# Kernel optimization log

Measured on AMD Instinct MI355X. Metric: run time of the kernel, lower is better.

The kernel has to match this reference:

```python
import jax, jax.numpy as jnp
import numpy as np

N_NODES = 100000
N_EDGES = 1600000
D_IN = 128
D_OUT = 32


def setup_inputs() -> dict:
    key = jax.random.key(0)
    k1, k2, k3 = jax.random.split(key, 3)
    x = jax.random.normal(k1, (N_NODES, D_IN), dtype=jnp.float32)
    edge_index = jax.random.randint(k2, (2, N_EDGES), 0, N_NODES, dtype=jnp.int64)
    W = jax.random.normal(k3, (D_IN, D_OUT), dtype=jnp.float32) * (1.0 / np.sqrt(D_IN))
    b = jnp.zeros((D_OUT,), dtype=jnp.float32)
    return {"x": x, "edge_index": edge_index, "W": W, "b": b}


def gcn_conv(x, edge_index, W, b):
    n = x.shape[0]
    # add self-loops (PyG GCNConv default)
    loops = jnp.arange(n, dtype=edge_index.dtype)
    row = jnp.concatenate([edge_index[0], loops])  # source
    col = jnp.concatenate([edge_index[1], loops])  # target
    # symmetric normalization: deg computed on target of A + I
    deg = jax.ops.segment_sum(jnp.ones_like(col, dtype=x.dtype), col, num_segments=n)
    dis = jnp.where(deg > 0, jax.lax.rsqrt(deg), 0.0)
    norm = dis[row] * dis[col]  # [E+N]
    # linear transform first, then gather-scale-scatter aggregation
    xw = x @ W  # [N, D_OUT]
    msgs = norm[:, None] * xw[row]  # [E+N, D_OUT]
    out = jax.ops.segment_sum(msgs, col, num_segments=n)
    return out + b


def reference(x, edge_index, W, b):
    return gcn_conv(x, edge_index, W, b)
```

## Files before the change

kernel.cpp:

```cpp
#include <hip/hip_runtime.h>

#define NN 100000
#define NE 1600000
#define DIN 128
#define DOUT 32
#define NBUK 391
#define FILLB 512
#define CHUNK 3125
#define CAP 8192
#define NTILES 6250
#define XWB 782

typedef unsigned short ushort_t;
typedef unsigned int uint_t;
typedef _Float16 f16x8 __attribute__((ext_vector_type(8)));
typedef float f32x4 __attribute__((ext_vector_type(4)));

static __device__ __forceinline__ ushort_t f2h_u(float f) {
    _Float16 h = (_Float16)f;
    ushort_t u;
    __builtin_memcpy(&u, &h, 2);
    return u;
}
static __device__ __forceinline__ float h2f(ushort_t us) {
    _Float16 h;
    __builtin_memcpy(&h, &us, 2);
    return (float)h;
}

__global__ __launch_bounds__(512)
void wb_zero_kernel(const float* __restrict__ W, ushort_t* __restrict__ Wht,
                    int* __restrict__ bsum) {
    if (blockIdx.x < 8) {
        int i = blockIdx.x * 512 + threadIdx.x;
        int c = i >> 7, k = i & 127;
        Wht[(size_t)c * DIN + k] = f2h_u(W[(size_t)k * DOUT + c]);
    } else {
        int t = threadIdx.x;
        if (t < NBUK) bsum[t] = 0;
    }
}

__global__ __launch_bounds__(512)
void fill_xw_kernel(const int* __restrict__ row, const int* __restrict__ col,
                    int* __restrict__ histmat, int* __restrict__ bsum,
                    unsigned int* __restrict__ records,
                    const float* __restrict__ x, const ushort_t* __restrict__ Wht,
                    ushort_t* __restrict__ xwsh) {
    __shared__ unsigned int stage[CHUNK];
    __shared__ int hist[NBUK];
    __shared__ int s[512];
    __shared__ int lcur[NBUK];
    if (blockIdx.x < FILLB) {
        int t = threadIdx.x, blk = blockIdx.x;
        for (int bb = t; bb < NBUK; bb += 512) hist[bb] = 0;
        __syncthreads();
        int e0 = blk * CHUNK;
        for (int j = t; j < CHUNK; j += 512) atomicAdd(&hist[col[e0 + j] >> 8], 1);
        __syncthreads();
        int own = (t < NBUK) ? hist[t] : 0;
        s[t] = own;
        __syncthreads();
        for (int off = 1; off < 512; off <<= 1) {
            int u = (t >= off) ? s[t - off] : 0;
            __syncthreads();
            s[t] += u;
            __syncthreads();
        }
        int excl = s[t] - own;
        if (t <= NBUK) histmat[(size_t)blk * (NBUK + 1) + t] = excl;
        if (t < NBUK) {
            if (own) atomicAdd(&bsum[t], own);
            lcur[t] = excl;
        }
        __syncthreads();
        for (int j = t; j < CHUNK; j += 512) {
            int e = e0 + j;
            int c = col[e];
            int slot = atomicAdd(&lcur[c >> 8], 1);
            stage[slot] = ((unsigned int)row[e] << 8) | (unsigned int)(c & 255);
        }
        __syncthreads();
        for (int j = t; j < CHUNK; j += 512)
            records[(size_t)blk * CHUNK + j] = stage[j];
        return;
    }
    int t = threadIdx.x;
    int wv = t >> 6, lane = t & 63;
    int wtile = (blockIdx.x - FILLB) * 8 + wv;
    if (wtile >= NTILES) return;
    int r0 = wtile * 16;
    int rowi = lane & 15;
    int kg = lane >> 4;

    f16x8 bfrag[2][4];
#pragma unroll
    for (int t2 = 0; t2 < 2; ++t2)
#pragma unroll
        for (int ss = 0; ss < 4; ++ss)
            bfrag[t2][ss] = *(const f16x8*)(Wht + (size_t)(t2 * 16 + rowi) * DIN + ss * 32 + kg * 8);

    const float* __restrict__ xr = x + (size_t)(r0 + rowi) * DIN;
    float4 xa[8];
#pragma unroll
    for (int ss = 0; ss < 4; ++ss) {
        xa[2 * ss]     = *(const float4*)(xr + ss * 32 + kg * 8);
        xa[2 * ss + 1] = *(const float4*)(xr + ss * 32 + kg * 8 + 4);
    }
    f16x8 afrag[4];
#pragma unroll
    for (int ss = 0; ss < 4; ++ss) {
        f16x8 a;
        a[0] = (_Float16)xa[2 * ss].x;     a[1] = (_Float16)xa[2 * ss].y;
        a[2] = (_Float16)xa[2 * ss].z;     a[3] = (_Float16)xa[2 * ss].w;
        a[4] = (_Float16)xa[2 * ss + 1].x; a[5] = (_Float16)xa[2 * ss + 1].y;
        a[6] = (_Float16)xa[2 * ss + 1].z; a[7] = (_Float16)xa[2 * ss + 1].w;
        afrag[ss] = a;
    }

    f32x4 acc0 = {0.f, 0.f, 0.f, 0.f};
    f32x4 acc1 = {0.f, 0.f, 0.f, 0.f};
#pragma unroll
    for (int ss = 0; ss < 4; ++ss) {
        acc0 = __builtin_amdgcn_mfma_f32_16x16x32_f16(afrag[ss], bfrag[0][ss], acc0, 0, 0, 0);
        acc1 = __builtin_amdgcn_mfma_f32_16x16x32_f16(afrag[ss], bfrag[1][ss], acc1, 0, 0, 0);
    }

#pragma unroll
    for (int j = 0; j < 4; ++j) {
        int orow = r0 + kg * 4 + j;
        xwsh[(size_t)orow * DOUT + rowi]      = f2h_u(acc0[j]);
        xwsh[(size_t)orow * DOUT + 16 + rowi] = f2h_u(acc1[j]);
    }
}

__global__ __launch_bounds__(512)
void bscan_kernel(const int* __restrict__ bsum, int* __restrict__ base) {
    __shared__ int s[512];
    int t = threadIdx.x;
    int own = (t < NBUK) ? bsum[t] : 0;
    s[t] = own;
    __syncthreads();
    for (int off = 1; off < 512; off <<= 1) {
        int v = (t >= off) ? s[t - off] : 0;
        __syncthreads();
        s[t] += v;
        __syncthreads();
    }
    if (t < NBUK) {
        base[t] = s[t] - own;
        if (t == NBUK - 1) base[NBUK] = s[t];
    }
}

__global__ __launch_bounds__(512)
void sort_kernel(const int* __restrict__ base, const int* __restrict__ histmat,
                 const unsigned int* __restrict__ records,
                 int* __restrict__ srcs, float* __restrict__ dis,
                 int* __restrict__ offs, ushort_t* __restrict__ xwsh) {
    __shared__ unsigned int stage[CAP];
    __shared__ int slen[512];
    __shared__ int hist[256];
    __shared__ int sc[256];
    __shared__ int lcur[256];
    __shared__ float disL[256];
    int b = blockIdx.x, t = threadIdx.x;
    int s_off = histmat[(size_t)t * (NBUK + 1) + b];
    int e_off = histmat[(size_t)t * (NBUK + 1) + b + 1];
    int len = e_off - s_off;
    slen[t] = len;
    if (t < 256) hist[t] = 0;
    __syncthreads();
    for (int off = 1; off < 512; off <<= 1) {
        int u = (t >= off) ? slen[t - off] : 0;
        __syncthreads();
        slen[t] += u;
        __syncthreads();
    }
    int pos = slen[t] - len;
    int cnt = slen[511];

    const unsigned int* seg = records + (size_t)t * CHUNK + s_off;
    for (int k = 0; k < len; k += 8) {
        unsigned int v[8];
#pragma unroll
        for (int u = 0; u < 8; ++u) {
            int idx = (k + u < len) ? (k + u) : (len - 1);
            v[u] = seg[idx];
        }
#pragma unroll
        for (int u = 0; u < 8; ++u)
            if (k + u < len) {
                stage[pos + k + u] = v[u];
                atomicAdd(&hist[v[u] & 255u], 1);
            }
    }
    __syncthreads();

    int d = (t < 256) ? hist[t] : 0;
    if (t < 256) sc[t] = d;
    __syncthreads();
    for (int off = 1; off < 256; off <<= 1) {
        int u = (t < 256 && t >= off) ? sc[t - off] : 0;
        __syncthreads();
        if (t < 256) sc[t] += u;
        __syncthreads();
    }
    int sbase = base[b];
    if (t < 256) {
        int excl = sc[t] - d;
        float dv = rsqrtf((float)(d + 1));
        disL[t] = dv;
        int n = (b << 8) + t;
        if (n < NN) {
            dis[n] = dv;
            offs[n] = sbase + excl;
            if (n == NN - 1) offs[NN] = sbase + cnt;
        }
        lcur[t] = excl;
    }
    __syncthreads();
    for (int j = t; j < cnt; j += 512) {
        unsigned int rec = stage[j];
        int slot = atomicAdd(&lcur[rec & 255u], 1);
        srcs[sbase + slot] = (int)(rec >> 8);
    }
    int n0 = b << 8;
    for (int idx = t; idx < 256 * 16; idx += 512) {
        int loc = idx >> 4;
        int n = n0 + loc;
        if (n >= NN) break;
        uint_t* p = (uint_t*)(xwsh + ((size_t)n << 5)) + (idx & 15);
        uint_t v = *p;
        float dv = disL[loc];
        float lo = h2f((ushort_t)(v & 0xffffu)) * dv;
        float hi = h2f((ushort_t)(v >> 16)) * dv;
        *p = (uint_t)f2h_u(lo) | ((uint_t)f2h_u(hi) << 16);
    }
}

__global__ __launch_bounds__(256)
void aggregate_kernel(const int* __restrict__ offs, const int* __restrict__ srcs,
                      const float* __restrict__ dis, const ushort_t* __restrict__ xwsh,
                      const float* __restrict__ bias, float* __restrict__ out) {
    int gw = (int)((blockIdx.x * (long long)blockDim.x + threadIdx.x) >> 6);
    int half = (threadIdx.x >> 5) & 1;
    int wid = gw * 2 + half;
    if (wid >= NN) return;
    int d = threadIdx.x & 31;

    int s = offs[wid], e = offs[wid + 1];
    float acc = h2f(xwsh[((size_t)wid << 5) + d]);
    for (int i = s; i < e; i += 8) {
        int r[8];
        ushort_t u[8];
#pragma unroll
        for (int k = 0; k < 8; ++k) {
            int j = i + k;
            r[k] = srcs[j < e ? j : e - 1];
        }
#pragma unroll
        for (int k = 0; k < 8; ++k) u[k] = xwsh[((size_t)r[k] << 5) + d];
#pragma unroll
        for (int k = 0; k < 8; ++k) acc += (i + k < e) ? h2f(u[k]) : 0.f;
    }
    out[((size_t)wid << 5) + d] = dis[wid] * acc + bias[d];
}

__global__ void deg_count_kernel(const int* __restrict__ col, int* __restrict__ deg) {
    int e = blockIdx.x * blockDim.x + threadIdx.x;
    if (e < NE) atomicAdd(&deg[col[e]], 1);
}
__global__ void dis_kernel(const int* __restrict__ deg, float* __restrict__ dis) {
    int i = blockIdx.x * blockDim.x + threadIdx.x;
    if (i < NN) dis[i] = rsqrtf((float)(deg[i] + 1));
}
__global__ void xw_init_kernel(const float* __restrict__ x, const float* __restrict__ W,
                               const float* __restrict__ b, const float* __restrict__ dis,
                               float* __restrict__ xw, float* __restrict__ out) {
    __shared__ float Ws[DIN * DOUT];
    for (int i = threadIdx.x; i < DIN * DOUT; i += blockDim.x) Ws[i] = W[i];
    __syncthreads();
    int idx = blockIdx.x * blockDim.x + threadIdx.x;
    if (idx >= NN * DOUT) return;
    int n = idx >> 5;
    int d = idx & (DOUT - 1);
    const float* xr = x + (long long)n * DIN;
    float acc = 0.f;
#pragma unroll
    for (int k = 0; k < DIN; ++k) acc += xr[k] * Ws[k * DOUT + d];
    xw[idx] = acc;
    float di = dis[n];
    out[idx] = di * di * acc + b[d];
}
__global__ void scatter_kernel(const int* __restrict__ row, const int* __restrict__ col,
                               const float* __restrict__ dis, const float* __restrict__ xw,
                               float* __restrict__ out) {
    long long idx = (long long)blockIdx.x * blockDim.x + threadIdx.x;
    if (idx >= (long long)NE * DOUT) return;
    int e = (int)(idx >> 5);
    int d = (int)(idx & (DOUT - 1));
    int r = row[e];
    int c = col[e];
    atomicAdd(&out[c * DOUT + d], dis[r] * dis[c] * xw[r * DOUT + d]);
}

extern "C" void kernel_launch(void* const* d_in, const int* in_sizes, int n_in,
                              void* d_out, int out_size, void* d_ws, size_t ws_size,
                              hipStream_t stream) {
    const float* x  = (const float*)d_in[0];
    const int*   ei = (const int*)d_in[1];
    const float* W  = (const float*)d_in[2];
    const float* b  = (const float*)d_in[3];
    float* out = (float*)d_out;

    const int* row = ei;
    const int* col = ei + NE;

    char* ws = (char*)d_ws;
    int*          histmat = (int*)(ws + 0);
    int*          bsum    = (int*)(ws + 802816);
    int*          base    = (int*)(ws + 804480);
    int*          offs    = (int*)(ws + 806144);
    float*        dis     = (float*)(ws + 1206272);
    unsigned int* records = (unsigned int*)(ws + 1606272);
    int*          srcs    = (int*)(ws + 8006272);
    ushort_t*     xwsh    = (ushort_t*)(ws + 14406272);
    ushort_t*     Wht     = (ushort_t*)(ws + 20806272);
    const size_t WS_NEEDED = 20814464ull;

    if (ws_size >= WS_NEEDED) {
        wb_zero_kernel<<<9, 512, 0, stream>>>(W, Wht, bsum);
        fill_xw_kernel<<<FILLB + XWB, 512, 0, stream>>>(row, col, histmat, bsum,
                                                        records, x, Wht, xwsh);
        bscan_kernel<<<1, 512, 0, stream>>>(bsum, base);
        sort_kernel<<<NBUK, 512, 0, stream>>>(base, histmat, records, srcs, dis, offs, xwsh);
        {
            long long waves = (NN + 1) / 2;
            int bl = (int)((waves + 3) / 4);
            aggregate_kernel<<<bl, 256, 0, stream>>>(offs, srcs, dis, xwsh, b, out);
        }
    } else {
        int* deg2 = (int*)(ws + 0);
        float* dis2 = (float*)(ws + 400128);
        float* xw = (float*)(ws + 800256);
        hipMemsetAsync(deg2, 0, NN * sizeof(int), stream);
        {
            int th = 256, bl = (NE + th - 1) / th;
            deg_count_kernel<<<bl, th, 0, stream>>>(col, deg2);
        }
        {
            int th = 256, bl = (NN + th - 1) / th;
            dis_kernel<<<bl, th, 0, stream>>>(deg2, dis2);
        }
        {
            long long total = (long long)NN * DOUT;
            int bl = (int)((total + 255) / 256);
            xw_init_kernel<<<bl, 256, 0, stream>>>(x, W, b, dis2, xw, out);
        }
        {
            long long total = (long long)NE * DOUT;
            int bl = (int)((total + 255) / 256);
            scatter_kernel<<<bl, 256, 0, stream>>>(row, col, dis2, xw, out);
        }
    }
}
```

Before: 90.44 us.

## Drop bucket-scan and W-prep kernels using padded per-bucket CSR segments

Result: faster. 76.05 us (-15.9%).

```diff
diff --git a/kernel.cpp b/kernel.cpp
--- a/kernel.cpp
+++ b/kernel.cpp
@@ -8,6 +8,7 @@
 #define FILLB 512
 #define CHUNK 3125
 #define CAP 8192
+#define CAP_PAD 4608
 #define NTILES 6250
 #define XWB 782
 
@@ -29,25 +30,12 @@
 }
 
 __global__ __launch_bounds__(512)
-void wb_zero_kernel(const float* __restrict__ W, ushort_t* __restrict__ Wht,
-                    int* __restrict__ bsum) {
-    if (blockIdx.x < 8) {
-        int i = blockIdx.x * 512 + threadIdx.x;
-        int c = i >> 7, k = i & 127;
-        Wht[(size_t)c * DIN + k] = f2h_u(W[(size_t)k * DOUT + c]);
-    } else {
-        int t = threadIdx.x;
-        if (t < NBUK) bsum[t] = 0;
-    }
-}
-
-__global__ __launch_bounds__(512)
 void fill_xw_kernel(const int* __restrict__ row, const int* __restrict__ col,
-                    int* __restrict__ histmat, int* __restrict__ bsum,
-                    unsigned int* __restrict__ records,
-                    const float* __restrict__ x, const ushort_t* __restrict__ Wht,
+                    int* __restrict__ histmat, unsigned int* __restrict__ records,
+                    const float* __restrict__ x, const float* __restrict__ W,
                     ushort_t* __restrict__ xwsh) {
     __shared__ unsigned int stage[CHUNK];
+    __shared__ int colstage[CHUNK];
     __shared__ int hist[NBUK];
     __shared__ int s[512];
     __shared__ int lcur[NBUK];
@@ -56,7 +44,11 @@
         for (int bb = t; bb < NBUK; bb += 512) hist[bb] = 0;
         __syncthreads();
         int e0 = blk * CHUNK;
-        for (int j = t; j < CHUNK; j += 512) atomicAdd(&hist[col[e0 + j] >> 8], 1);
+        for (int j = t; j < CHUNK; j += 512) {
+            int c = col[e0 + j];
+            colstage[j] = c;
+            atomicAdd(&hist[c >> 8], 1);
+        }
         __syncthreads();
         int own = (t < NBUK) ? hist[t] : 0;
         s[t] = own;
@@ -69,16 +61,12 @@
         }
         int excl = s[t] - own;
         if (t <= NBUK) histmat[(size_t)blk * (NBUK + 1) + t] = excl;
-        if (t < NBUK) {
-            if (own) atomicAdd(&bsum[t], own);
-            lcur[t] = excl;
-        }
+        if (t < NBUK) lcur[t] = excl;
         __syncthreads();
         for (int j = t; j < CHUNK; j += 512) {
-            int e = e0 + j;
-            int c = col[e];
+            int c = colstage[j];
             int slot = atomicAdd(&lcur[c >> 8], 1);
-            stage[slot] = ((unsigned int)row[e] << 8) | (unsigned int)(c & 255);
+            stage[slot] = ((unsigned int)row[e0 + j] << 8) | (unsigned int)(c & 255);
         }
         __syncthreads();
         for (int j = t; j < CHUNK; j += 512)
@@ -95,10 +83,17 @@
 
     f16x8 bfrag[2][4];
 #pragma unroll
-    for (int t2 = 0; t2 < 2; ++t2)
-#pragma unroll
-        for (int ss = 0; ss < 4; ++ss)
-            bfrag[t2][ss] = *(const f16x8*)(Wht + (size_t)(t2 * 16 + rowi) * DIN + ss * 32 + kg * 8);
+    for (int t2 = 0; t2 < 2; ++t2) {
+        int c = t2 * 16 + rowi;
+#pragma unroll
+        for (int ss = 0; ss < 4; ++ss) {
+            const float* Wp = W + (size_t)(ss * 32 + kg * 8) * DOUT + c;
+            f16x8 bf;
+#pragma unroll
+            for (int i = 0; i < 8; ++i) bf[i] = (_Float16)Wp[i * DOUT];
+            bfrag[t2][ss] = bf;
+        }
+    }
 
     const float* __restrict__ xr = x + (size_t)(r0 + rowi) * DIN;
     float4 xa[8];
@@ -135,29 +130,11 @@
 }
 
 __global__ __launch_bounds__(512)
-void bscan_kernel(const int* __restrict__ bsum, int* __restrict__ base) {
-    __shared__ int s[512];
-    int t = threadIdx.x;
-    int own = (t < NBUK) ? bsum[t] : 0;
-    s[t] = own;
-    __syncthreads();
-    for (int off = 1; off < 512; off <<= 1) {
-        int v = (t >= off) ? s[t - off] : 0;
-        __syncthreads();
-        s[t] += v;
-        __syncthreads();
-    }
-    if (t < NBUK) {
-        base[t] = s[t] - own;
-        if (t == NBUK - 1) base[NBUK] = s[t];
-    }
-}
-
-__global__ __launch_bounds__(512)
-void sort_kernel(const int* __restrict__ base, const int* __restrict__ histmat,
+void sort_kernel(const int* __restrict__ histmat,
                  const unsigned int* __restrict__ records,
                  int* __restrict__ srcs, float* __restrict__ dis,
-                 int* __restrict__ offs, ushort_t* __restrict__ xwsh) {
+                 int* __restrict__ offs, int* __restrict__ ends,
+                 ushort_t* __restrict__ xwsh) {
     __shared__ unsigned int stage[CAP];
     __shared__ int slen[512];
     __shared__ int hist[256];
@@ -206,7 +183,7 @@
         if (t < 256) sc[t] += u;
         __syncthreads();
     }
-    int sbase = base[b];
+    int sbase = b * CAP_PAD;
     if (t < 256) {
         int excl = sc[t] - d;
         float dv = rsqrtf((float)(d + 1));
@@ -215,7 +192,7 @@
         if (n < NN) {
             dis[n] = dv;
             offs[n] = sbase + excl;
-            if (n == NN - 1) offs[NN] = sbase + cnt;
+            ends[n] = sbase + sc[t];
         }
         lcur[t] = excl;
     }
@@ -240,7 +217,8 @@
 }
 
 __global__ __launch_bounds__(256)
-void aggregate_kernel(const int* __restrict__ offs, const int* __restrict__ srcs,
+void aggregate_kernel(const int* __restrict__ offs, const int* __restrict__ ends,
+                      const int* __restrict__ srcs,
                       const float* __restrict__ dis, const ushort_t* __restrict__ xwsh,
                       const float* __restrict__ bias, float* __restrict__ out) {
     int gw = (int)((blockIdx.x * (long long)blockDim.x + threadIdx.x) >> 6);
@@ -249,7 +227,7 @@
     if (wid >= NN) return;
     int d = threadIdx.x & 31;
 
-    int s = offs[wid], e = offs[wid + 1];
+    int s = offs[wid], e = ends[wid];
     float acc = h2f(xwsh[((size_t)wid << 5) + d]);
     for (int i = s; i < e; i += 8) {
         int r[8];
@@ -319,26 +297,23 @@
 
     char* ws = (char*)d_ws;
     int*          histmat = (int*)(ws + 0);
-    int*          bsum    = (int*)(ws + 802816);
-    int*          base    = (int*)(ws + 804480);
-    int*          offs    = (int*)(ws + 806144);
-    float*        dis     = (float*)(ws + 1206272);
-    unsigned int* records = (unsigned int*)(ws + 1606272);
-    int*          srcs    = (int*)(ws + 8006272);
-    ushort_t*     xwsh    = (ushort_t*)(ws + 14406272);
-    ushort_t*     Wht     = (ushort_t*)(ws + 20806272);
-    const size_t WS_NEEDED = 20814464ull;
+    int*          offs    = (int*)(ws + 802816);
+    int*          ends    = (int*)(ws + 1202816);
+    float*        dis     = (float*)(ws + 1602816);
+    unsigned int* records = (unsigned int*)(ws + 2002816);
+    int*          srcs    = (int*)(ws + 8402816);
+    ushort_t*     xwsh    = (ushort_t*)(ws + 15609728);
+    const size_t WS_NEEDED = 22009728ull;
 
     if (ws_size >= WS_NEEDED) {
-        wb_zero_kernel<<<9, 512, 0, stream>>>(W, Wht, bsum);
-        fill_xw_kernel<<<FILLB + XWB, 512, 0, stream>>>(row, col, histmat, bsum,
-                                                        records, x, Wht, xwsh);
-        bscan_kernel<<<1, 512, 0, stream>>>(bsum, base);
-        sort_kernel<<<NBUK, 512, 0, stream>>>(base, histmat, records, srcs, dis, offs, xwsh);
+        fill_xw_kernel<<<FILLB + XWB, 512, 0, stream>>>(row, col, histmat,
+                                                        records, x, W, xwsh);
+        sort_kernel<<<NBUK, 512, 0, stream>>>(histmat, records, srcs, dis,
+                                              offs, ends, xwsh);
         {
             long long waves = (NN + 1) / 2;
             int bl = (int)((waves + 3) / 4);
-            aggregate_kernel<<<bl, 256, 0, stream>>>(offs, srcs, dis, xwsh, b, out);
+            aggregate_kernel<<<bl, 256, 0, stream>>>(offs, ends, srcs, dis, xwsh, b, out);
         }
     } else {
         int* deg2 = (int*)(ws + 0);
```
